# Optimization experiments

Measured on AMD Instinct MI355X. Metric: run time of the kernel, lower is better.

The kernel has to match this reference:

```python
import jax, jax.numpy as jnp
import numpy as np

B, N, DE, DH, L, DC = 8, 256, 768, 192, 2, 192
NEG = 1e30  # mask_logic constant from the repo


def setup_inputs() -> dict:
    ks = iter(jax.random.split(jax.random.key(0), 32))

    def nrm(shape, s=0.02):
        return jax.random.normal(next(ks), shape, dtype=jnp.float32) * s

    features = jax.random.normal(next(ks), (B, N, DE), dtype=jnp.float32)
    # DAG adjacency: node i attends to a subset of j < i; guarantee edge (i, i-1)
    rnd = jax.random.bernoulli(next(ks), 0.3, (B, N, N))
    tril = jnp.tril(jnp.ones((N, N), jnp.bool_), -1)
    adj = ((rnd & tril[None]) | jnp.eye(N, k=-1, dtype=jnp.bool_)[None]).astype(jnp.float32)
    s_mask = jax.random.bernoulli(next(ks), 0.5, (B, N, N)).astype(jnp.float32)
    s_mask_onehot = jnp.stack([1.0 - s_mask, s_mask], axis=-1)  # unused in forward
    lengths = jnp.full((B,), N, dtype=jnp.int32)  # unused (nodal_att_type=None)
    return dict(
        features=features, adj=adj, s_mask=s_mask,
        s_mask_onehot=s_mask_onehot, lengths=lengths,
        fc1_w=nrm((DE, DH)), fc1_b=jnp.zeros((DH,), jnp.float32),
        gat_w=nrm((L, 2 * DH)), gat_b=jnp.zeros((L,), jnp.float32),
        wr0=nrm((L, DH, DH)), wr1=nrm((L, DH, DH)),
        gruc_wih=nrm((L, 3 * DH, DH)), gruc_whh=nrm((L, 3 * DH, DH)),
        gruc_bih=jnp.zeros((L, 3 * DH), jnp.float32),
        gruc_bhh=jnp.zeros((L, 3 * DH), jnp.float32),
        grup_wih=nrm((L, 3 * DH, DH)), grup_whh=nrm((L, 3 * DH, DH)),
        grup_bih=jnp.zeros((L, 3 * DH), jnp.float32),
        grup_bhh=jnp.zeros((L, 3 * DH), jnp.float32),
        mlp_w0=nrm((DH * (L + 1), DH)), mlp_b0=jnp.zeros((DH,), jnp.float32),
        mlp_w1=nrm((DH, DH)), mlp_b1=jnp.zeros((DH,), jnp.float32),
        mlp_w2=nrm((DH, DC)), mlp_b2=jnp.zeros((DC,), jnp.float32),
    )


def _gru(x, h, wih, whh, bih, bhh):
    # torch.nn.GRUCell math
    gi = x @ wih.T + bih
    gh = h @ whh.T + bhh
    ir, iz, inn = jnp.split(gi, 3, axis=-1)
    hr, hz, hn = jnp.split(gh, 3, axis=-1)
    r = jax.nn.sigmoid(ir + hr)
    z = jax.nn.sigmoid(iz + hz)
    n = jnp.tanh(inn + r * hn)
    return (1.0 - z) * n + z * h


def _layer(Hl, adj, s_mask, gat_w, gat_b, wr0, wr1, cw, cp):
    # One DAG layer: sequential scan over nodes. Carry holds the relation-
    # projected value buffers V0=H1@Wr0^T, V1=H1@Wr1^T and per-node key
    # scores Ksc=H1@wk (rows >= i are zero and masked out), which is
    # mathematically identical to the torch code that re-projects the
    # growing H1 every step.
    wq, wk = gat_w[:DH], gat_w[DH:]
    pos = jnp.arange(N)

    def step(carry, xs):
        V0, V1, Ksc = carry
        i, x_i, adj_i, sm_i = xs  # x_i:(B,DH) adj_i,sm_i:(B,N)
        score = (x_i @ wq)[:, None] + Ksc + gat_b          # (B,N)
        mask = (pos < i)[None, :] & (adj_i > 0.5)          # ragged :i slice
        alpha = jnp.where(mask, score, score - NEG)        # mask_logic
        attn = jax.nn.softmax(alpha, axis=-1)              # masked -> exactly 0
        Vrel = V0 * sm_i[..., None] + V1 * (1.0 - sm_i[..., None])
        M = jnp.einsum('bn,bnd->bd', attn, Vrel)
        M = jnp.where(i > 0, M, 0.0)                       # node 0: no context
        C = _gru(x_i, M, *cw)
        P = _gru(M, x_i, *cp)
        Hnew = C + P
        V0 = V0.at[:, i, :].set(Hnew @ wr0.T)
        V1 = V1.at[:, i, :].set(Hnew @ wr1.T)
        Ksc = Ksc.at[:, i].set(Hnew @ wk)
        attn_out = jnp.where(i > 0, attn, 0.0)             # adjB row 0 is zeros
        return (V0, V1, Ksc), (Hnew, attn_out)

    z3 = jnp.zeros((B, N, DH), jnp.float32)
    carry0 = (z3, z3, jnp.zeros((B, N), jnp.float32))
    xs = (pos, Hl.transpose(1, 0, 2), adj.transpose(1, 0, 2), s_mask.transpose(1, 0, 2))
    _, (Hseq, Aseq) = jax.lax.scan(step, carry0, xs)
    return Hseq.transpose(1, 0, 2), Aseq.transpose(1, 0, 2)  # (B,N,DH),(B,N,N)


def reference(features, adj, s_mask, s_mask_onehot, lengths,
              fc1_w, fc1_b, gat_w, gat_b, wr0, wr1,
              gruc_wih, gruc_whh, gruc_bih, gruc_bhh,
              grup_wih, grup_whh, grup_bih, grup_bhh,
              mlp_w0, mlp_b0, mlp_w1, mlp_b1, mlp_w2, mlp_b2):
    Hl = jax.nn.relu(features @ fc1_w + fc1_b)  # H0
    Hs, As = [Hl], []
    for l in range(L):
        cw = (gruc_wih[l], gruc_whh[l], gruc_bih[l], gruc_bhh[l])
        cp = (grup_wih[l], grup_whh[l], grup_bih[l], grup_bhh[l])
        Hl, Al = _layer(Hl, adj, s_mask, gat_w[l], gat_b[l], wr0[l], wr1[l], cw, cp)
        Hs.append(Hl)
        As.append(Al)
    H = jnp.concatenate(Hs, axis=2)  # (B,N,DH*(L+1))
    # nodal_att_type=None => attentive_node_features is identity
    h = jax.nn.relu(H @ mlp_w0 + mlp_b0)
    h = jax.nn.relu(h @ mlp_w1 + mlp_b1)  # mlp_layers-1 = 1 extra block
    logits = h @ mlp_w2 + mlp_b2          # dropout: eval-mode identity
    return logits, jnp.stack(As, axis=1)  # (B,N,DC), (B,L,N,N)
```

## Files before the change

### kernel.cpp

```cpp
#include <hip/hip_runtime.h>
#include <stdint.h>

#define B_  8
#define N_  256
#define DH_ 192
#define L_  2
#define G3  576
#define G6  1152
#define NW  4
#define DS  48
#define KD  24
#define GC  288
#define STH 10001
#define STP 20001
#define STQ 25001

typedef unsigned long long u64;

__device__ __forceinline__ float bflo(uint32_t u) { return __uint_as_float(u << 16); }
__device__ __forceinline__ float bfhi(uint32_t u) { return __uint_as_float(u & 0xffff0000u); }
__device__ __forceinline__ uint32_t f2bf(float f) {
    uint32_t x = __float_as_uint(f);
    x += 0x7fffu + ((x >> 16) & 1u);
    return x >> 16;
}
__device__ __forceinline__ float sigm(float x)  { return 1.f / (1.f + __expf(-x)); }
__device__ __forceinline__ float tanhf_(float x){ return 1.f - 2.f / (1.f + __expf(2.f * x)); }
__device__ __forceinline__ u64 packvs(float v, int st) {
    return ((u64)(uint32_t)st << 32) | __float_as_uint(v);
}
__device__ __forceinline__ u64 agload(const u64* p) {
    return __hip_atomic_load(p, __ATOMIC_RELAXED, __HIP_MEMORY_SCOPE_AGENT);
}
__device__ __forceinline__ void agstore(u64* p, u64 v) {
    __hip_atomic_store(p, v, __ATOMIC_RELAXED, __HIP_MEMORY_SCOPE_AGENT);
}

__global__ void prepack_kernel(
    const float* __restrict__ wr0, const float* __restrict__ wr1,
    const float* __restrict__ c_wih, const float* __restrict__ c_whh,
    const float* __restrict__ c_bih, const float* __restrict__ c_bhh,
    const float* __restrict__ p_wih, const float* __restrict__ p_whh,
    const float* __restrict__ p_bih, const float* __restrict__ p_bhh,
    float* __restrict__ WpreT, uint32_t* __restrict__ W4,
    uint32_t* __restrict__ Wr4, uint32_t* __restrict__ Wp4w,
    float* __restrict__ biasPre, float* __restrict__ gbx)
{
    int idx = blockIdx.x * blockDim.x + threadIdx.x;
    if (idx >= DH_ * G6) return;
    for (int l = 0; l < L_; ++l) {
        const float* cwih = c_wih + l * G3 * DH_;
        const float* cwhh = c_whh + l * G3 * DH_;
        const float* pwih = p_wih + l * G3 * DH_;
        const float* pwhh = p_whh + l * G3 * DH_;
        if (l == 0) {
            int k = idx / G6, r = idx - k * G6;
            float w = (r < G3) ? cwih[r * DH_ + k] : pwhh[(r - G3) * DH_ + k];
            WpreT[k * G6 + r] = w;
        }
        if (idx < NW * 27648) {
            int w = idx / 27648, pos = idx % 27648;
            int p4 = pos / 1152, rem = pos % 1152;
            int c2 = rem >> 2, s = rem & 3;
            int p = 4 * p4 + s;
            int j = c2 / DS, dd = c2 % DS;
            int c = 192 * j + DS * w + dd;
            float w0 = (c < G3) ? cwhh[c * DH_ + 2 * p]     : pwih[(c - G3) * DH_ + 2 * p];
            float w1 = (c < G3) ? cwhh[c * DH_ + 2 * p + 1] : pwih[(c - G3) * DH_ + 2 * p + 1];
            W4[l * NW * 27648 + idx] = f2bf(w0) | (f2bf(w1) << 16);
            if (l == 1) {
                int r = 192 * j + DS * w + dd;
                float v0 = (r < G3) ? cwih[r * DH_ + 2 * p]     : pwhh[(r - G3) * DH_ + 2 * p];
                float v1 = (r < G3) ? cwih[r * DH_ + 2 * p + 1] : pwhh[(r - G3) * DH_ + 2 * p + 1];
                Wp4w[idx] = f2bf(v0) | (f2bf(v1) << 16);
            }
        }
        if (idx < NW * 9216) {
            int w = idx / 9216, pos = idx % 9216;
            int kq = pos / 768, rem = pos % 768;
            int d = rem >> 2, s = rem & 3;
            int k = DS * w + 4 * kq + s;
            Wr4[l * NW * 9216 + idx] =
                f2bf(wr0[l * DH_ * DH_ + d * DH_ + k]) |
                (f2bf(wr1[l * DH_ * DH_ + d * DH_ + k]) << 16);
        }
        if (idx < G6) {
            float base = (idx < G3) ? c_bih[l * G3 + idx] : p_bhh[l * G3 + idx - G3];
            float fold = 0.f;
            if (idx < 384)                    fold = c_bhh[l * G3 + idx];
            else if (idx >= G3 && idx < 960)  fold = p_bih[l * G3 + idx - G3];
            biasPre[l * G6 + idx] = base + fold;
        }
        if (idx < 384) {
            gbx[l * 384 + idx] = (idx < DH_) ? c_bhh[l * G3 + 384 + idx]
                                             : p_bih[l * G3 + 384 + (idx - DH_)];
        }
    }
}

#define GR 8
__global__ __launch_bounds__(192) void gemm_kernel(
    const float* __restrict__ A, int lda, const float* __restrict__ Bm,
    const float* __restrict__ bias, float* __restrict__ C, int ldc,
    int K, int cols, int relu)
{
    __shared__ float sA[GR][64];
    const int c  = blockIdx.y * 192 + threadIdx.x;
    const int r0 = blockIdx.x * GR;
    float acc[GR] = {0.f, 0.f, 0.f, 0.f, 0.f, 0.f, 0.f, 0.f};
    for (int k0 = 0; k0 < K; k0 += 64) {
        for (int idx = threadIdx.x; idx < GR * 64; idx += 192) {
            int rr = idx >> 6, kk = idx & 63;
            sA[rr][kk] = A[(size_t)(r0 + rr) * lda + k0 + kk];
        }
        __syncthreads();
        #pragma unroll 8
        for (int kk = 0; kk < 64; ++kk) {
            float bv = Bm[(size_t)(k0 + kk) * cols + c];
            #pragma unroll
            for (int rr = 0; rr < GR; ++rr) acc[rr] += sA[rr][kk] * bv;
        }
        __syncthreads();
    }
    float bv = bias[c];
    #pragma unroll
    for (int rr = 0; rr < GR; ++rr) {
        float v = acc[rr] + bv;
        if (relu) v = fmaxf(v, 0.f);
        C[(size_t)(r0 + rr) * ldc + c] = v;
    }
}

struct ScanSm {
    uint4 Wlds4[24 * GC];
    uint4 Wr4s[12 * DH_];
    float sA0[N_], sA1[N_], sKsc[N_];
    float sAdjN[N_], sSmN[N_];
    float sXq[DH_], sPre[6 * DS], sXv[DS];
    float sM[DH_], su0[DS], su1[DS], sGc[GC], sHn[DS];
    float sRedS[4], sRedX[3], sSaved[4];
};
struct WorkSm {
    uint4 Wp4[24 * GC];
    float sX[DH_];
    float sPv[GC];
    float sRed[3];
};

template<int ISL2>
__device__ void scan_body(
    ScanSm* S, int b, int w, int t,
    const float* __restrict__ xin, float* __restrict__ hout,
    const float* __restrict__ PREg, const float* __restrict__ adj,
    const float* __restrict__ smask,
    const uint32_t* __restrict__ W4l, const uint32_t* __restrict__ Wr4l,
    const float* __restrict__ gbxl, const float* __restrict__ gatwl,
    uint32_t* __restrict__ Hw, u64* __restrict__ MPsl, u64* __restrict__ Kdl,
    u64* __restrict__ HcW, const u64* __restrict__ HcR,
    const u64* __restrict__ PREcR, const u64* __restrict__ XQcR,
    float* __restrict__ AsB, int sbase)
{
    const int lane = t & 63, wave = t >> 6;
    const int dg0 = w * DS;
    const float* adjB = adj   + (size_t)b * N_ * N_;
    const float* smB  = smask + (size_t)b * N_ * N_;
    const int fi = b * NW;

    {
        uint32_t* wl = (uint32_t*)S->Wlds4;
        for (int q = t; q < 27648; q += 576) wl[q] = W4l[q];
        uint32_t* wr = (uint32_t*)S->Wr4s;
        for (int q = t; q < 9216; q += 576) wr[q] = Wr4l[q];
    }
    float wqv = (!ISL2 && t < DH_) ? gatwl[t] : 0.f;
    float wkv = 0.f, g2b = 0.f, g5b = 0.f;
    if (t < DS) { wkv = gatwl[DH_ + dg0 + t]; g2b = gbxl[dg0 + t]; g5b = gbxl[DH_ + dg0 + t]; }
    if (t < N_) S->sKsc[t] = 0.f;
    if (w == 0 && t < N_) AsB[t] = 0.f;

    if (!ISL2) {
        if (t < DS) {
            const float* pre = PREg + (size_t)(b * N_) * G6 + dg0 + t;
            S->sPre[t] = pre[0]; S->sPre[DS + t] = pre[192]; S->sPre[2 * DS + t] = pre[384];
            S->sPre[3 * DS + t] = pre[576]; S->sPre[4 * DS + t] = pre[768]; S->sPre[5 * DS + t] = pre[960];
            S->sXv[t] = xin[(size_t)(b * N_) * G3 + dg0 + t];
        }
        for (int q = t; q < 176; q += 576) {
            if (q < 64)       *(float4*)&S->sAdjN[4 * q] = *(const float4*)(adjB + N_ + 4 * q);
            else if (q < 128) { int q2 = q - 64;  *(float4*)&S->sSmN[4 * q2] = *(const float4*)(smB + N_ + 4 * q2); }
            else              { int q2 = q - 128; *(float4*)&S->sXq[4 * q2] = *(const float4*)(xin + (size_t)(b * N_ + 1) * G3 + 4 * q2); }
        }
    } else {
        for (int q = t; q < 321; q += 576) {
            if (q < 64)       *(float4*)&S->sAdjN[4 * q] = *(const float4*)(adjB + N_ + 4 * q);
            else if (q < 128) { int q2 = q - 64;  *(float4*)&S->sSmN[4 * q2] = *(const float4*)(smB + N_ + 4 * q2); }
            else if (q < 176) {
                int d = q - 128;
                const u64* p = HcR + ((size_t)(b * N_) * NW + w) * DS + d;
                u64 v; do { v = agload(p); } while ((uint32_t)(v >> 32) != (uint32_t)STH);
                S->sXv[d] = __uint_as_float((uint32_t)v);
            } else if (q < 320) {
                int qq = q - 176;
                const u64* p = PREcR + ((size_t)(b * N_) * NW + w) * 144 + qq;
                u64 v; do { v = agload(p); } while ((uint32_t)(v >> 32) != (uint32_t)STP);
                uint32_t pl = (uint32_t)v;
                S->sPre[2 * qq] = bflo(pl); S->sPre[2 * qq + 1] = bfhi(pl);
            } else {
                const u64* p = XQcR + b * N_ + 1;
                u64 v; do { v = agload(p); } while ((uint32_t)(v >> 32) != (uint32_t)(STQ + 1));
                S->sSaved[3] = __uint_as_float((uint32_t)v);
            }
        }
    }
    __syncthreads();
    {
        float hn = 0.f;
        if (t < DS) {
            float xv = S->sXv[t];
            float r1 = sigm(S->sPre[t]), z1 = sigm(S->sPre[DS + t]);
            float n1 = tanhf_(S->sPre[2 * DS + t] + r1 * g2b);
            float Cv = (1.f - z1) * n1;
            float r2 = sigm(S->sPre[3 * DS + t]), z2 = sigm(S->sPre[4 * DS + t]);
            float n2 = tanhf_(g5b + r2 * S->sPre[5 * DS + t]);
            hn = Cv + (1.f - z2) * n2 + z2 * xv;
            S->sHn[t] = hn;
            hout[(size_t)(b * N_) * G3 + dg0 + t] = hn;
            if (!ISL2) HcW[((size_t)(b * N_) * NW + w) * DS + t] = packvs(hn, STH);
        }
        if (wave == 0) {
            float v = hn * wkv;
            #pragma unroll
            for (int o = 32; o; o >>= 1) v += __shfl_xor(v, o);
            if (lane == 0) agstore(&Kdl[fi + w], packvs(v, sbase));
        }
    }
    __syncthreads();
    if (t < KD) Hw[(size_t)t * N_] = f2bf(S->sHn[2 * t]) | (f2bf(S->sHn[2 * t + 1]) << 16);
    if (!ISL2) {
        float px = (t < DH_) ? S->sXq[t] * wqv : 0.f;
        #pragma unroll
        for (int o = 32; o; o >>= 1) px += __shfl_xor(px, o);
        if (t < DH_ && lane == 0) S->sRedX[wave] = px;
    }
    __syncthreads();
    float xq = ISL2 ? S->sSaved[3] : (S->sRedX[0] + S->sRedX[1] + S->sRedX[2]);

    for (int i = 1; i < N_; ++i) {
        const int row = b * N_ + i;
        const int stamp = sbase + i;
        {
            float e = 0.f;
            if (t == i - 1) { S->sSaved[0] = S->sAdjN[t]; S->sSaved[1] = S->sSmN[t]; }
            if (t < N_) {
                if (t < i - 1 && S->sAdjN[t] > 0.5f) e = __expf(xq + S->sKsc[t]);
                float b0 = e * S->sSmN[t];
                S->sA0[t] = b0; S->sA1[t] = e - b0;
            }
            float ps = e;
            #pragma unroll
            for (int o = 32; o; o >>= 1) ps += __shfl_xor(ps, o);
            if (t < N_ && lane == 0) S->sRedS[wave] = ps;
        }
        __syncthreads();
        if (t < 384) {
            const int ilim = i - 1;
            const int kd = t >> 4, jp = t & 15;
            const uint32_t* hp = Hw + (size_t)kd * N_;
            float u0l = 0.f, u0h = 0.f, u1l = 0.f, u1h = 0.f;
            int j = jp;
            while (j + 48 < ilim) {
                uint32_t h0 = hp[j], h1 = hp[j + 16], h2 = hp[j + 32], h3 = hp[j + 48];
                float b0, b1;
                b0 = S->sA0[j];      b1 = S->sA1[j];
                u0l = fmaf(b0, bflo(h0), u0l); u0h = fmaf(b0, bfhi(h0), u0h);
                u1l = fmaf(b1, bflo(h0), u1l); u1h = fmaf(b1, bfhi(h0), u1h);
                b0 = S->sA0[j + 16]; b1 = S->sA1[j + 16];
                u0l = fmaf(b0, bflo(h1), u0l); u0h = fmaf(b0, bfhi(h1), u0h);
                u1l = fmaf(b1, bflo(h1), u1l); u1h = fmaf(b1, bfhi(h1), u1h);
                b0 = S->sA0[j + 32]; b1 = S->sA1[j + 32];
                u0l = fmaf(b0, bflo(h2), u0l); u0h = fmaf(b0, bfhi(h2), u0h);
                u1l = fmaf(b1, bflo(h2), u1l); u1h = fmaf(b1, bfhi(h2), u1h);
                b0 = S->sA0[j + 48]; b1 = S->sA1[j + 48];
                u0l = fmaf(b0, bflo(h3), u0l); u0h = fmaf(b0, bfhi(h3), u0h);
                u1l = fmaf(b1, bflo(h3), u1l); u1h = fmaf(b1, bfhi(h3), u1h);
                j += 64;
            }
            for (; j < ilim; j += 16) {
                uint32_t hv = hp[j];
                float b0 = S->sA0[j], b1 = S->sA1[j];
                u0l = fmaf(b0, bflo(hv), u0l); u0h = fmaf(b0, bfhi(hv), u0h);
                u1l = fmaf(b1, bflo(hv), u1l); u1h = fmaf(b1, bfhi(hv), u1h);
            }
            #pragma unroll
            for (int o = 1; o <= 8; o <<= 1) {
                u0l += __shfl_xor(u0l, o); u0h += __shfl_xor(u0h, o);
                u1l += __shfl_xor(u1l, o); u1h += __shfl_xor(u1h, o);
            }
            if (jp == 0) {
                S->su0[2 * kd] = u0l; S->su0[2 * kd + 1] = u0h;
                S->su1[2 * kd] = u1l; S->su1[2 * kd + 1] = u1h;
            }
        } else {
            const int u = t - 384;
            const int inx = (i + 1 < N_) ? i + 1 : N_ - 1;
            if (!ISL2) {
                for (int q = u; q < 260; q += 192) {
                    if (q < 64)
                        *(float4*)&S->sAdjN[4 * q] = *(const float4*)(adjB + (size_t)inx * N_ + 4 * q);
                    else if (q < 128) { int q2 = q - 64;
                        *(float4*)&S->sSmN[4 * q2] = *(const float4*)(smB + (size_t)inx * N_ + 4 * q2); }
                    else if (q < 140) { int q2 = q - 128;
                        *(float4*)&S->sXv[4 * q2] = *(const float4*)(xin + (size_t)row * G3 + dg0 + 4 * q2); }
                    else if (q < 212) { int q2 = q - 140; int g = q2 / 12, o = q2 - 12 * g;
                        *(float4*)&S->sPre[g * DS + 4 * o] =
                            *(const float4*)(PREg + (size_t)row * G6 + g * DH_ + dg0 + 4 * o); }
                    else { int q2 = q - 212;
                        *(float4*)&S->sXq[4 * q2] = *(const float4*)(xin + (size_t)(b * N_ + inx) * G3 + 4 * q2); }
                }
            } else {
                for (int q = u; q < 321; q += 192) {
                    if (q < 64)
                        *(float4*)&S->sAdjN[4 * q] = *(const float4*)(adjB + (size_t)inx * N_ + 4 * q);
                    else if (q < 128) { int q2 = q - 64;
                        *(float4*)&S->sSmN[4 * q2] = *(const float4*)(smB + (size_t)inx * N_ + 4 * q2); }
                    else if (q < 176) {
                        int d = q - 128;
                        const u64* p = HcR + ((size_t)row * NW + w) * DS + d;
                        u64 v; do { v = agload(p); } while ((uint32_t)(v >> 32) != (uint32_t)(STH + i));
                        S->sXv[d] = __uint_as_float((uint32_t)v);
                    } else if (q < 320) {
                        int qq = q - 176;
                        const u64* p = PREcR + ((size_t)row * NW + w) * 144 + qq;
                        u64 v; do { v = agload(p); } while ((uint32_t)(v >> 32) != (uint32_t)(STP + i));
                        uint32_t pl = (uint32_t)v;
                        S->sPre[2 * qq] = bflo(pl); S->sPre[2 * qq + 1] = bfhi(pl);
                    } else {
                        const u64* p = XQcR + b * N_ + inx;
                        u64 v; do { v = agload(p); } while ((uint32_t)(v >> 32) != (uint32_t)(STQ + inx));
                        S->sSaved[3] = __uint_as_float((uint32_t)v);
                    }
                }
            }
            if (t == 575) {
                const uint32_t ex = (uint32_t)(stamp - 1);
                u64 k0, k1, k2, k3;
                do {
                    k0 = agload(&Kdl[fi + 0]); k1 = agload(&Kdl[fi + 1]);
                    k2 = agload(&Kdl[fi + 2]); k3 = agload(&Kdl[fi + 3]);
                } while ((uint32_t)(k0 >> 32) != ex || (uint32_t)(k1 >> 32) != ex ||
                         (uint32_t)(k2 >> 32) != ex || (uint32_t)(k3 >> 32) != ex);
                float kdot = __uint_as_float((uint32_t)k0) + __uint_as_float((uint32_t)k1)
                           + __uint_as_float((uint32_t)k2) + __uint_as_float((uint32_t)k3);
                float adjI1 = S->sSaved[0], smI1 = S->sSaved[1];
                float e1 = (adjI1 > 0.5f) ? __expf(xq + kdot) : 0.f;
                float Ssum = S->sRedS[0] + S->sRedS[1] + S->sRedS[2] + S->sRedS[3] + e1;
                S->sKsc[i - 1] = kdot;
                float c0 = e1 * smI1;
                S->sA0[i - 1] = c0; S->sA1[i - 1] = e1 - c0;
                S->sSaved[2] = 1.f / Ssum;
            }
        }
        __syncthreads();
        if (t < DH_) {
            float mp = 0.f, h0a = 0.f, h1a = 0.f;
            #pragma unroll 4
            for (int kq = 0; kq < 12; ++kq) {
                uint4 wv = S->Wr4s[kq * DH_ + t];
                const int k0 = 4 * kq;
                float lo, hi;
                lo = bflo(wv.x); hi = bfhi(wv.x);
                mp = fmaf(S->su0[k0 + 0], lo, mp); mp = fmaf(S->su1[k0 + 0], hi, mp);
                h0a = fmaf(S->sHn[k0 + 0], lo, h0a); h1a = fmaf(S->sHn[k0 + 0], hi, h1a);
                lo = bflo(wv.y); hi = bfhi(wv.y);
                mp = fmaf(S->su0[k0 + 1], lo, mp); mp = fmaf(S->su1[k0 + 1], hi, mp);
                h0a = fmaf(S->sHn[k0 + 1], lo, h0a); h1a = fmaf(S->sHn[k0 + 1], hi, h1a);
                lo = bflo(wv.z); hi = bfhi(wv.z);
                mp = fmaf(S->su0[k0 + 2], lo, mp); mp = fmaf(S->su1[k0 + 2], hi, mp);
                h0a = fmaf(S->sHn[k0 + 2], lo, h0a); h1a = fmaf(S->sHn[k0 + 2], hi, h1a);
                lo = bflo(wv.w); hi = bfhi(wv.w);
                mp = fmaf(S->su0[k0 + 3], lo, mp); mp = fmaf(S->su1[k0 + 3], hi, mp);
                h0a = fmaf(S->sHn[k0 + 3], lo, h0a); h1a = fmaf(S->sHn[k0 + 3], hi, h1a);
            }
            float invS = S->sSaved[2];
            mp = (mp + S->sA0[i - 1] * h0a + S->sA1[i - 1] * h1a) * invS;
            agstore(&MPsl[(size_t)(fi + w) * DH_ + t], packvs(mp, stamp));
            const int w1 = (w + 1) & 3, w2 = (w + 2) & 3, w3 = (w + 3) & 3;
            u64* pA = &MPsl[(size_t)(fi + w1) * DH_ + t];
            u64* pB = &MPsl[(size_t)(fi + w2) * DH_ + t];
            u64* pC = &MPsl[(size_t)(fi + w3) * DH_ + t];
            const uint32_t ex = (uint32_t)stamp;
            u64 vA, vB, vC;
            do {
                vA = agload(pA); vB = agload(pB); vC = agload(pC);
            } while ((uint32_t)(vA >> 32) != ex || (uint32_t)(vB >> 32) != ex ||
                     (uint32_t)(vC >> 32) != ex);
            S->sM[t] = mp + __uint_as_float((uint32_t)vA)
                          + __uint_as_float((uint32_t)vB)
                          + __uint_as_float((uint32_t)vC);
        } else if (w == 0 && t < 448) {
            int j = t - 192;
            AsB[(size_t)i * N_ + j] = (S->sA0[j] + S->sA1[j]) * S->sSaved[2];
        }
        __syncthreads();
        {
            const int c = t >> 1, kh = t & 1;
            const uint4* wp = S->Wlds4 + (12 * kh) * GC + c;
            float g = 0.f;
            #pragma unroll 4
            for (int p4 = 0; p4 < 12; ++p4) {
                uint4 wv = wp[p4 * GC];
                const int m0 = 8 * (12 * kh + p4);
                g = fmaf(S->sM[m0 + 0], bflo(wv.x), g); g = fmaf(S->sM[m0 + 1], bfhi(wv.x), g);
                g = fmaf(S->sM[m0 + 2], bflo(wv.y), g); g = fmaf(S->sM[m0 + 3], bfhi(wv.y), g);
                g = fmaf(S->sM[m0 + 4], bflo(wv.z), g); g = fmaf(S->sM[m0 + 5], bfhi(wv.z), g);
                g = fmaf(S->sM[m0 + 6], bflo(wv.w), g); g = fmaf(S->sM[m0 + 7], bfhi(wv.w), g);
            }
            g += __shfl_xor(g, 1);
            if (kh == 0) S->sGc[c] = g;
        }
        __syncthreads();
        {
            float hn = 0.f;
            if (t < DS) {
                float Mv = S->sM[dg0 + t];
                float r1 = sigm(S->sPre[t] + S->sGc[t]);
                float z1 = sigm(S->sPre[DS + t] + S->sGc[DS + t]);
                float n1 = tanhf_(S->sPre[2 * DS + t] + r1 * (S->sGc[2 * DS + t] + g2b));
                float Cv = (1.f - z1) * n1 + z1 * Mv;
                float r2 = sigm(S->sGc[3 * DS + t] + S->sPre[3 * DS + t]);
                float z2 = sigm(S->sGc[4 * DS + t] + S->sPre[4 * DS + t]);
                float n2 = tanhf_(S->sGc[5 * DS + t] + g5b + r2 * S->sPre[5 * DS + t]);
                hn = Cv + (1.f - z2) * n2 + z2 * S->sXv[t];
                S->sHn[t] = hn;
                hout[(size_t)row * G3 + dg0 + t] = hn;
                if (!ISL2) HcW[((size_t)row * NW + w) * DS + t] = packvs(hn, STH + i);
            }
            if (wave == 0) {
                float v = hn * wkv;
                #pragma unroll
                for (int o = 32; o; o >>= 1) v += __shfl_xor(v, o);
                if (lane == 0) agstore(&Kdl[fi + w], packvs(v, stamp));
            }
            if (t < KD) Hw[(size_t)t * N_ + i] = f2bf(S->sHn[2 * t]) | (f2bf(S->sHn[2 * t + 1]) << 16);
            if (!ISL2) {
                float px = (t < DH_) ? S->sXq[t] * wqv : 0.f;
                #pragma unroll
                for (int o = 32; o; o >>= 1) px += __shfl_xor(px, o);
                if (t < DH_ && lane == 0) S->sRedX[wave] = px;
            }
        }
        __syncthreads();
        xq = ISL2 ? S->sSaved[3] : (S->sRedX[0] + S->sRedX[1] + S->sRedX[2]);
    }
}

__device__ void worker_body(WorkSm* Wm, int b, int w, int t,
    const uint32_t* __restrict__ Wp4g, const float* __restrict__ bias2,
    const float* __restrict__ wq2,
    const u64* __restrict__ HcR, u64* __restrict__ PREcW, u64* __restrict__ XQcW)
{
    const int lane = t & 63, wave = t >> 6;
    { uint32_t* wl = (uint32_t*)Wm->Wp4; for (int q = t; q < 27648; q += 576) wl[q] = Wp4g[q]; }
    const int c = t >> 1, kh = t & 1;
    float bv = 0.f;
    if (kh == 0) bv = bias2[192 * (c / DS) + w * DS + (c % DS)];
    float wqt = (t < DH_) ? wq2[t] : 0.f;
    for (int i = 0; i < N_; ++i) {
        if (t < DH_) {
            const u64* p = HcR + ((size_t)(b * N_ + i) * NW + (t / DS)) * DS + (t % DS);
            u64 v; do { v = agload(p); } while ((uint32_t)(v >> 32) != (uint32_t)(STH + i));
            Wm->sX[t] = __uint_as_float((uint32_t)v);
        }
        __syncthreads();
        {
            const uint4* wp = Wm->Wp4 + (12 * kh) * GC + c;
            float g = 0.f;
            #pragma unroll 4
            for (int p4 = 0; p4 < 12; ++p4) {
                uint4 wv = wp[p4 * GC];
                const int m0 = 8 * (12 * kh + p4);
                g = fmaf(Wm->sX[m0 + 0], bflo(wv.x), g); g = fmaf(Wm->sX[m0 + 1], bfhi(wv.x), g);
                g = fmaf(Wm->sX[m0 + 2], bflo(wv.y), g); g = fmaf(Wm->sX[m0 + 3], bfhi(wv.y), g);
                g = fmaf(Wm->sX[m0 + 4], bflo(wv.z), g); g = fmaf(Wm->sX[m0 + 5], bfhi(wv.z), g);
                g = fmaf(Wm->sX[m0 + 6], bflo(wv.w), g); g = fmaf(Wm->sX[m0 + 7], bfhi(wv.w), g);
            }
            g += __shfl_xor(g, 1);
            if (kh == 0) Wm->sPv[c] = g + bv;
        }
        if (w == 0) {
            float px = (t < DH_) ? Wm->sX[t] * wqt : 0.f;
            #pragma unroll
            for (int o = 32; o; o >>= 1) px += __shfl_xor(px, o);
            if (t < DH_ && lane == 0) Wm->sRed[wave] = px;
        }
        __syncthreads();
        if (t < 144) {
            u64 v = ((u64)(uint32_t)(STP + i) << 32)
                  | f2bf(Wm->sPv[2 * t]) | (f2bf(Wm->sPv[2 * t + 1]) << 16);
            agstore(&PREcW[((size_t)(b * N_ + i) * NW + w) * 144 + t], v);
        }
        if (w == 0 && t == 0)
            agstore(&XQcW[b * N_ + i],
                    packvs(Wm->sRed[0] + Wm->sRed[1] + Wm->sRed[2], STQ + i));
        __syncthreads();
    }
}

__global__ __launch_bounds__(576, 1) void pipeline_kernel(
    float* __restrict__ Hcat, const float* __restrict__ PREg,
    const float* __restrict__ adj, const float* __restrict__ smask,
    const uint32_t* __restrict__ W4, const uint32_t* __restrict__ Wr4,
    const uint32_t* __restrict__ Wp4w,
    const float* __restrict__ biasPre, const float* __restrict__ gbx,
    const float* __restrict__ gatw,
    uint32_t* __restrict__ Hb, u64* __restrict__ MPs, u64* __restrict__ Kd,
    u64* __restrict__ Hc, u64* __restrict__ PREc, u64* __restrict__ XQc,
    float* __restrict__ As)
{
    __shared__ __align__(16) char smem[sizeof(ScanSm)];
    const int blk = blockIdx.x, t = threadIdx.x;
    const int b = blk & 7, r12 = blk >> 3;
    const int role = r12 >> 2, w = r12 & 3;
    if (role == 0) {
        scan_body<0>((ScanSm*)smem, b, w, t,
            Hcat, Hcat + 192, PREg, adj, smask,
            W4, Wr4, gbx, gatw,
            Hb + (size_t)(b * NW + w) * KD * N_, MPs, Kd,
            Hc, nullptr, nullptr, nullptr,
            As + (size_t)b * (L_ * N_ * N_), 1);
    } else if (role == 2) {
        scan_body<1>((ScanSm*)smem, b, w, t,
            nullptr, Hcat + 384, nullptr, adj, smask,
            W4 + NW * 27648, Wr4 + NW * 9216, gbx + 384, gatw + 384,
            Hb + (size_t)(32 + b * NW + w) * KD * N_,
            MPs + (size_t)8 * NW * DH_, Kd + 8 * NW,
            nullptr, Hc, PREc, XQc,
            As + (size_t)b * (L_ * N_ * N_) + N_ * N_, 30001);
    } else {
        worker_body((WorkSm*)smem, b, w, t,
            Wp4w + (size_t)w * 27648, biasPre + G6, gatw + 384,
            Hc, PREc, XQc);
    }
}

extern "C" void kernel_launch(void* const* d_in, const int* in_sizes, int n_in,
                              void* d_out, int out_size, void* d_ws, size_t ws_size,
                              hipStream_t stream)
{
    const float* features = (const float*)d_in[0];
    const float* adj      = (const float*)d_in[1];
    const float* smask    = (const float*)d_in[2];
    const float* fc1_w = (const float*)d_in[5];
    const float* fc1_b = (const float*)d_in[6];
    const float* gat_w = (const float*)d_in[7];
    const float* wr0   = (const float*)d_in[9];
    const float* wr1   = (const float*)d_in[10];
    const float* c_wih = (const float*)d_in[11];
    const float* c_whh = (const float*)d_in[12];
    const float* c_bih = (const float*)d_in[13];
    const float* c_bhh = (const float*)d_in[14];
    const float* p_wih = (const float*)d_in[15];
    const float* p_whh = (const float*)d_in[16];
    const float* p_bih = (const float*)d_in[17];
    const float* p_bhh = (const float*)d_in[18];
    const float* mw0 = (const float*)d_in[19];
    const float* mb0 = (const float*)d_in[20];
    const float* mw1 = (const float*)d_in[21];
    const float* mb1 = (const float*)d_in[22];
    const float* mw2 = (const float*)d_in[23];
    const float* mb2 = (const float*)d_in[24];
    float* out = (float*)d_out;

    char* wsb = (char*)d_ws;
    size_t off = 0;
    auto carve = [&](size_t bytes) -> char* {
        char* p = wsb + off;
        off = (off + bytes + 255) & ~(size_t)255;
        return p;
    };
    float* Hcat     = (float*)carve(2048ull * 576 * 4);
    float* PREg     = (float*)carve(2048ull * 1152 * 4);
    float* WpreT    = (float*)carve(192ull * 1152 * 4);
    uint32_t* W4    = (uint32_t*)carve(2ull * NW * 27648 * 4);
    uint32_t* Wr4   = (uint32_t*)carve(2ull * NW * 9216 * 4);
    uint32_t* Wp4w  = (uint32_t*)carve((size_t)NW * 27648 * 4);
    float* biasPre  = (float*)carve(2ull * 1152 * 4);
    float* gbx      = (float*)carve(2ull * 384 * 4);
    uint32_t* Hb    = (uint32_t*)carve(64ull * KD * 256 * 4);
    u64* MPs        = (u64*)carve(2ull * 8 * NW * DH_ * 8);
    u64* Kd         = (u64*)carve(2ull * 8 * NW * 8);
    u64* Hc         = (u64*)carve(8ull * 256 * NW * DS * 8);
    u64* PREc       = (u64*)carve(8ull * 256 * NW * 144 * 8);
    u64* XQc        = (u64*)carve(8ull * 256 * 8);
    float* h1 = PREg;
    float* h2 = PREg + 2048 * 192;

    prepack_kernel<<<dim3((192 * 1152 + 255) / 256), 256, 0, stream>>>(
        wr0, wr1, c_wih, c_whh, c_bih, c_bhh, p_wih, p_whh, p_bih, p_bhh,
        WpreT, W4, Wr4, Wp4w, biasPre, gbx);

    gemm_kernel<<<dim3(256, 1), 192, 0, stream>>>(features, 768, fc1_w, fc1_b,
                                                  Hcat, 576, 768, 192, 1);
    gemm_kernel<<<dim3(256, 6), 192, 0, stream>>>(Hcat, 576,
        WpreT, biasPre, PREg, 1152, 192, 1152, 0);

    pipeline_kernel<<<dim3(96), 576, 0, stream>>>(
        Hcat, PREg, adj, smask, W4, Wr4, Wp4w, biasPre, gbx, gat_w,
        Hb, MPs, Kd, Hc, PREc, XQc, out + 393216);

    gemm_kernel<<<dim3(256, 1), 192, 0, stream>>>(Hcat, 576, mw0, mb0, h1, 192, 576, 192, 1);
    gemm_kernel<<<dim3(256, 1), 192, 0, stream>>>(h1, 192, mw1, mb1, h2, 192, 192, 192, 1);
    gemm_kernel<<<dim3(256, 1), 192, 0, stream>>>(h2, 192, mw2, mb2, out, 192, 192, 192, 0);
}
```

Before: 2.006 ms.

## Fuse prepack, prologue GEMMs and MLP tail into single persistent pipeline kernel

Merges the weight-prepack kernel, the fc1 and pre-activation GEMMs, and the three MLP GEMMs into the persistent 96-block pipeline kernel. Phases are separated by software grid barriers built on stamped flags in global memory. The MLP tail waits on per-scan completion flags. The goal is to remove five kernel launches and their gaps, at the cost of spin-wait grid barriers that need all 96 blocks resident at once, and GEMMs that now run on only 96 workgroups.

```diff
diff --git a/kernel.cpp b/kernel.cpp
--- a/kernel.cpp
+++ b/kernel.cpp
@@ -14,6 +14,10 @@
 #define STH 10001
 #define STP 20001
 #define STQ 25001
+#define SPK 50000
+#define SF1 50001
+#define SF2 50002
+#define SDN 60001
 
 typedef unsigned long long u64;
 
@@ -34,101 +38,6 @@
 }
 __device__ __forceinline__ void agstore(u64* p, u64 v) {
     __hip_atomic_store(p, v, __ATOMIC_RELAXED, __HIP_MEMORY_SCOPE_AGENT);
-}
-
-__global__ void prepack_kernel(
-    const float* __restrict__ wr0, const float* __restrict__ wr1,
-    const float* __restrict__ c_wih, const float* __restrict__ c_whh,
-    const float* __restrict__ c_bih, const float* __restrict__ c_bhh,
-    const float* __restrict__ p_wih, const float* __restrict__ p_whh,
-    const float* __restrict__ p_bih, const float* __restrict__ p_bhh,
-    float* __restrict__ WpreT, uint32_t* __restrict__ W4,
-    uint32_t* __restrict__ Wr4, uint32_t* __restrict__ Wp4w,
-    float* __restrict__ biasPre, float* __restrict__ gbx)
-{
-    int idx = blockIdx.x * blockDim.x + threadIdx.x;
-    if (idx >= DH_ * G6) return;
-    for (int l = 0; l < L_; ++l) {
-        const float* cwih = c_wih + l * G3 * DH_;
-        const float* cwhh = c_whh + l * G3 * DH_;
-        const float* pwih = p_wih + l * G3 * DH_;
-        const float* pwhh = p_whh + l * G3 * DH_;
-        if (l == 0) {
-            int k = idx / G6, r = idx - k * G6;
-            float w = (r < G3) ? cwih[r * DH_ + k] : pwhh[(r - G3) * DH_ + k];
-            WpreT[k * G6 + r] = w;
-        }
-        if (idx < NW * 27648) {
-            int w = idx / 27648, pos = idx % 27648;
-            int p4 = pos / 1152, rem = pos % 1152;
-            int c2 = rem >> 2, s = rem & 3;
-            int p = 4 * p4 + s;
-            int j = c2 / DS, dd = c2 % DS;
-            int c = 192 * j + DS * w + dd;
-            float w0 = (c < G3) ? cwhh[c * DH_ + 2 * p]     : pwih[(c - G3) * DH_ + 2 * p];
-            float w1 = (c < G3) ? cwhh[c * DH_ + 2 * p + 1] : pwih[(c - G3) * DH_ + 2 * p + 1];
-            W4[l * NW * 27648 + idx] = f2bf(w0) | (f2bf(w1) << 16);
-            if (l == 1) {
-                int r = 192 * j + DS * w + dd;
-                float v0 = (r < G3) ? cwih[r * DH_ + 2 * p]     : pwhh[(r - G3) * DH_ + 2 * p];
-                float v1 = (r < G3) ? cwih[r * DH_ + 2 * p + 1] : pwhh[(r - G3) * DH_ + 2 * p + 1];
-                Wp4w[idx] = f2bf(v0) | (f2bf(v1) << 16);
-            }
-        }
-        if (idx < NW * 9216) {
-            int w = idx / 9216, pos = idx % 9216;
-            int kq = pos / 768, rem = pos % 768;
-            int d = rem >> 2, s = rem & 3;
-            int k = DS * w + 4 * kq + s;
-            Wr4[l * NW * 9216 + idx] =
-                f2bf(wr0[l * DH_ * DH_ + d * DH_ + k]) |
-                (f2bf(wr1[l * DH_ * DH_ + d * DH_ + k]) << 16);
-        }
-        if (idx < G6) {
-            float base = (idx < G3) ? c_bih[l * G3 + idx] : p_bhh[l * G3 + idx - G3];
-            float fold = 0.f;
-            if (idx < 384)                    fold = c_bhh[l * G3 + idx];
-            else if (idx >= G3 && idx < 960)  fold = p_bih[l * G3 + idx - G3];
-            biasPre[l * G6 + idx] = base + fold;
-        }
-        if (idx < 384) {
-            gbx[l * 384 + idx] = (idx < DH_) ? c_bhh[l * G3 + 384 + idx]
-                                             : p_bih[l * G3 + 384 + (idx - DH_)];
-        }
-    }
-}
-
-#define GR 8
-__global__ __launch_bounds__(192) void gemm_kernel(
-    const float* __restrict__ A, int lda, const float* __restrict__ Bm,
-    const float* __restrict__ bias, float* __restrict__ C, int ldc,
-    int K, int cols, int relu)
-{
-    __shared__ float sA[GR][64];
-    const int c  = blockIdx.y * 192 + threadIdx.x;
-    const int r0 = blockIdx.x * GR;
-    float acc[GR] = {0.f, 0.f, 0.f, 0.f, 0.f, 0.f, 0.f, 0.f};
-    for (int k0 = 0; k0 < K; k0 += 64) {
-        for (int idx = threadIdx.x; idx < GR * 64; idx += 192) {
-            int rr = idx >> 6, kk = idx & 63;
-            sA[rr][kk] = A[(size_t)(r0 + rr) * lda + k0 + kk];
-        }
-        __syncthreads();
-        #pragma unroll 8
-        for (int kk = 0; kk < 64; ++kk) {
-            float bv = Bm[(size_t)(k0 + kk) * cols + c];
-            #pragma unroll
-            for (int rr = 0; rr < GR; ++rr) acc[rr] += sA[rr][kk] * bv;
-        }
-        __syncthreads();
-    }
-    float bv = bias[c];
-    #pragma unroll
-    for (int rr = 0; rr < GR; ++rr) {
-        float v = acc[rr] + bv;
-        if (relu) v = fmaxf(v, 0.f);
-        C[(size_t)(r0 + rr) * ldc + c] = v;
-    }
 }
 
 struct ScanSm {
@@ -146,6 +55,248 @@
     float sPv[GC];
     float sRed[3];
 };
+struct PrologSm {
+    float sA[8][768];
+    float sRed[3][8][192];
+};
+struct MlpSm {
+    float sH[8][576];
+    float sRed[3][8][192];
+    float sT[8][192];
+};
+
+__device__ void prepack_slice(int idx,
+    const float* __restrict__ wr0, const float* __restrict__ wr1,
+    const float* __restrict__ c_wih, const float* __restrict__ c_whh,
+    const float* __restrict__ c_bih, const float* __restrict__ c_bhh,
+    const float* __restrict__ p_wih, const float* __restrict__ p_whh,
+    const float* __restrict__ p_bih, const float* __restrict__ p_bhh,
+    float* __restrict__ WpreT, uint32_t* __restrict__ W4,
+    uint32_t* __restrict__ Wr4, uint32_t* __restrict__ Wp4w,
+    float* __restrict__ biasPre, float* __restrict__ gbx)
+{
+    for (int l = 0; l < L_; ++l) {
+        const float* cwih = c_wih + l * G3 * DH_;
+        const float* cwhh = c_whh + l * G3 * DH_;
+        const float* pwih = p_wih + l * G3 * DH_;
+        const float* pwhh = p_whh + l * G3 * DH_;
+        if (l == 0) {
+            int k = idx / G6, r = idx - k * G6;
+            float w = (r < G3) ? cwih[r * DH_ + k] : pwhh[(r - G3) * DH_ + k];
+            WpreT[k * G6 + r] = w;
+        }
+        if (idx < NW * 27648) {
+            int w = idx / 27648, pos = idx % 27648;
+            int p4 = pos / 1152, rem = pos % 1152;
+            int c2 = rem >> 2, s = rem & 3;
+            int p = 4 * p4 + s;
+            int j = c2 / DS, dd = c2 % DS;
+            int c = 192 * j + DS * w + dd;
+            float w0 = (c < G3) ? cwhh[c * DH_ + 2 * p]     : pwih[(c - G3) * DH_ + 2 * p];
+            float w1 = (c < G3) ? cwhh[c * DH_ + 2 * p + 1] : pwih[(c - G3) * DH_ + 2 * p + 1];
+            W4[l * NW * 27648 + idx] = f2bf(w0) | (f2bf(w1) << 16);
+            if (l == 1) {
+                int r = c;
+                float v0 = (r < G3) ? cwih[r * DH_ + 2 * p]     : pwhh[(r - G3) * DH_ + 2 * p];
+                float v1 = (r < G3) ? cwih[r * DH_ + 2 * p + 1] : pwhh[(r - G3) * DH_ + 2 * p + 1];
+                Wp4w[idx] = f2bf(v0) | (f2bf(v1) << 16);
+            }
+        }
+        if (idx < NW * 9216) {
+            int w = idx / 9216, pos = idx % 9216;
+            int kq = pos / 768, rem = pos % 768;
+            int d = rem >> 2, s = rem & 3;
+            int k = DS * w + 4 * kq + s;
+            Wr4[l * NW * 9216 + idx] =
+                f2bf(wr0[l * DH_ * DH_ + d * DH_ + k]) |
+                (f2bf(wr1[l * DH_ * DH_ + d * DH_ + k]) << 16);
+        }
+        if (idx < G6) {
+            float base = (idx < G3) ? c_bih[l * G3 + idx] : p_bhh[l * G3 + idx - G3];
+            float fold = 0.f;
+            if (idx < 384)                    fold = c_bhh[l * G3 + idx];
+            else if (idx >= G3 && idx < 960)  fold = p_bih[l * G3 + idx - G3];
+            biasPre[l * G6 + idx] = base + fold;
+        }
+        if (idx < 384) {
+            gbx[l * 384 + idx] = (idx < DH_) ? c_bhh[l * G3 + 384 + idx]
+                                             : p_bih[l * G3 + 384 + (idx - DH_)];
+        }
+    }
+}
+
+__device__ void flag_sync(u64* flags, int wgid, int t, int stamp)
+{
+    __threadfence();
+    __syncthreads();
+    if (t == 0) agstore(&flags[wgid], packvs(0.f, stamp));
+    if (t < 96) {
+        while ((uint32_t)(agload(&flags[t]) >> 32) != (uint32_t)stamp) {}
+    }
+    __syncthreads();
+    __threadfence();
+    __syncthreads();
+}
+
+__device__ void prologue(char* smem, int wgid, int t,
+    const float* __restrict__ features, const float* __restrict__ fc1_w,
+    const float* __restrict__ fc1_b, const float* __restrict__ WpreT,
+    const float* __restrict__ biasPre,
+    float* __restrict__ Hcat, float* __restrict__ PREg, u64* __restrict__ Fp)
+{
+    PrologSm* P = (PrologSm*)smem;
+    const int c = t % 192, kg = t / 192;
+    for (int tt = wgid; tt < 256; tt += 96) {
+        const int r0 = tt * 8;
+        for (int q = t; q < 1536; q += 576) {
+            int r = q / 192, c4 = q % 192;
+            *(float4*)&P->sA[r][4 * c4] = *(const float4*)(features + (size_t)(r0 + r) * 768 + 4 * c4);
+        }
+        __syncthreads();
+        {
+            const float* bp = fc1_w + (size_t)(kg * 256) * 192 + c;
+            float acc[8] = {0.f, 0.f, 0.f, 0.f, 0.f, 0.f, 0.f, 0.f};
+            #pragma unroll 8
+            for (int kk = 0; kk < 256; ++kk) {
+                float bv = bp[(size_t)kk * 192];
+                #pragma unroll
+                for (int rr = 0; rr < 8; ++rr) acc[rr] += P->sA[rr][kg * 256 + kk] * bv;
+            }
+            #pragma unroll
+            for (int rr = 0; rr < 8; ++rr) P->sRed[kg][rr][c] = acc[rr];
+        }
+        __syncthreads();
+        if (t < 192) {
+            float bv = fc1_b[t];
+            #pragma unroll
+            for (int rr = 0; rr < 8; ++rr) {
+                float v = P->sRed[0][rr][t] + P->sRed[1][rr][t] + P->sRed[2][rr][t] + bv;
+                Hcat[(size_t)(r0 + rr) * G3 + t] = fmaxf(v, 0.f);
+            }
+        }
+        __syncthreads();
+    }
+    flag_sync(Fp + 96, wgid, t, SF1);
+    {
+        const float bpa = biasPre[t], bpb = biasPre[576 + t];
+        for (int tt = wgid; tt < 256; tt += 96) {
+            const int r0 = tt * 8;
+            for (int q = t; q < 384; q += 576) {
+                int r = q / 48, c4 = q % 48;
+                *(float4*)&P->sA[r][4 * c4] = *(const float4*)(Hcat + (size_t)(r0 + r) * G3 + 4 * c4);
+            }
+            __syncthreads();
+            {
+                const float* b0 = WpreT + t;
+                float a0[8] = {0.f,0.f,0.f,0.f,0.f,0.f,0.f,0.f};
+                float a1[8] = {0.f,0.f,0.f,0.f,0.f,0.f,0.f,0.f};
+                #pragma unroll 4
+                for (int k = 0; k < 192; ++k) {
+                    float bva = b0[(size_t)k * G6];
+                    float bvb = b0[(size_t)k * G6 + 576];
+                    #pragma unroll
+                    for (int rr = 0; rr < 8; ++rr) {
+                        float av = P->sA[rr][k];
+                        a0[rr] += av * bva; a1[rr] += av * bvb;
+                    }
+                }
+                #pragma unroll
+                for (int rr = 0; rr < 8; ++rr) {
+                    PREg[(size_t)(r0 + rr) * G6 + t]       = a0[rr] + bpa;
+                    PREg[(size_t)(r0 + rr) * G6 + 576 + t] = a1[rr] + bpb;
+                }
+            }
+            __syncthreads();
+        }
+    }
+    flag_sync(Fp + 192, wgid, t, SF2);
+}
+
+__device__ void mlp_tail(char* smem, int wgid, int t,
+    const float* __restrict__ Hcat,
+    const float* __restrict__ mw0, const float* __restrict__ mb0,
+    const float* __restrict__ mw1, const float* __restrict__ mb1,
+    const float* __restrict__ mw2, const float* __restrict__ mb2,
+    float* __restrict__ out, u64* __restrict__ Fd)
+{
+    if (t < 64) {
+        while ((uint32_t)(agload(&Fd[t]) >> 32) != (uint32_t)SDN) {}
+    }
+    __syncthreads();
+    __threadfence();
+    __syncthreads();
+    MlpSm* M = (MlpSm*)smem;
+    const int c = t % 192, kg = t / 192;
+    for (int tt = wgid; tt < 256; tt += 96) {
+        const int r0 = tt * 8;
+        for (int q = t; q < 1152; q += 576) {
+            int r = q / 144, c4 = q % 144;
+            *(float4*)&M->sH[r][4 * c4] = *(const float4*)(Hcat + (size_t)(r0 + r) * G3 + 4 * c4);
+        }
+        __syncthreads();
+        {
+            const float* bp = mw0 + (size_t)(kg * 192) * 192 + c;
+            float acc[8] = {0.f,0.f,0.f,0.f,0.f,0.f,0.f,0.f};
+            #pragma unroll 8
+            for (int kk = 0; kk < 192; ++kk) {
+                float bv = bp[(size_t)kk * 192];
+                #pragma unroll
+                for (int rr = 0; rr < 8; ++rr) acc[rr] += M->sH[rr][kg * 192 + kk] * bv;
+            }
+            #pragma unroll
+            for (int rr = 0; rr < 8; ++rr) M->sRed[kg][rr][c] = acc[rr];
+        }
+        __syncthreads();
+        if (t < 192) {
+            float bv = mb0[t];
+            #pragma unroll
+            for (int rr = 0; rr < 8; ++rr)
+                M->sT[rr][t] = fmaxf(M->sRed[0][rr][t] + M->sRed[1][rr][t] + M->sRed[2][rr][t] + bv, 0.f);
+        }
+        __syncthreads();
+        {
+            const float* bp = mw1 + (size_t)(kg * 64) * 192 + c;
+            float acc[8] = {0.f,0.f,0.f,0.f,0.f,0.f,0.f,0.f};
+            #pragma unroll 8
+            for (int kk = 0; kk < 64; ++kk) {
+                float bv = bp[(size_t)kk * 192];
+                #pragma unroll
+                for (int rr = 0; rr < 8; ++rr) acc[rr] += M->sT[rr][kg * 64 + kk] * bv;
+            }
+            #pragma unroll
+            for (int rr = 0; rr < 8; ++rr) M->sRed[kg][rr][c] = acc[rr];
+        }
+        __syncthreads();
+        if (t < 192) {
+            float bv = mb1[t];
+            #pragma unroll
+            for (int rr = 0; rr < 8; ++rr)
+                M->sH[rr][t] = fmaxf(M->sRed[0][rr][t] + M->sRed[1][rr][t] + M->sRed[2][rr][t] + bv, 0.f);
+        }
+        __syncthreads();
+        {
+            const float* bp = mw2 + (size_t)(kg * 64) * 192 + c;
+            float acc[8] = {0.f,0.f,0.f,0.f,0.f,0.f,0.f,0.f};
+            #pragma unroll 8
+            for (int kk = 0; kk < 64; ++kk) {
+                float bv = bp[(size_t)kk * 192];
+                #pragma unroll
+                for (int rr = 0; rr < 8; ++rr) acc[rr] += M->sH[rr][kg * 64 + kk] * bv;
+            }
+            #pragma unroll
+            for (int rr = 0; rr < 8; ++rr) M->sRed[kg][rr][c] = acc[rr];
+        }
+        __syncthreads();
+        if (t < 192) {
+            float bv = mb2[t];
+            #pragma unroll
+            for (int rr = 0; rr < 8; ++rr)
+                out[(size_t)(r0 + rr) * 192 + t] =
+                    M->sRed[0][rr][t] + M->sRed[1][rr][t] + M->sRed[2][rr][t] + bv;
+        }
+        __syncthreads();
+    }
+}
 
 template<int ISL2>
 __device__ void scan_body(
@@ -507,20 +658,45 @@
 }
 
 __global__ __launch_bounds__(576, 1) void pipeline_kernel(
-    float* __restrict__ Hcat, const float* __restrict__ PREg,
+    const float* __restrict__ features, const float* __restrict__ fc1_w,
+    const float* __restrict__ fc1_b,
     const float* __restrict__ adj, const float* __restrict__ smask,
-    const uint32_t* __restrict__ W4, const uint32_t* __restrict__ Wr4,
-    const uint32_t* __restrict__ Wp4w,
-    const float* __restrict__ biasPre, const float* __restrict__ gbx,
     const float* __restrict__ gatw,
+    const float* __restrict__ wr0, const float* __restrict__ wr1,
+    const float* __restrict__ c_wih, const float* __restrict__ c_whh,
+    const float* __restrict__ c_bih, const float* __restrict__ c_bhh,
+    const float* __restrict__ p_wih, const float* __restrict__ p_whh,
+    const float* __restrict__ p_bih, const float* __restrict__ p_bhh,
+    const float* __restrict__ mw0, const float* __restrict__ mb0,
+    const float* __restrict__ mw1, const float* __restrict__ mb1,
+    const float* __restrict__ mw2, const float* __restrict__ mb2,
+    float* __restrict__ Hcat, float* __restrict__ PREg,
+    float* __restrict__ WpreT, uint32_t* __restrict__ W4,
+    uint32_t* __restrict__ Wr4, uint32_t* __restrict__ Wp4w,
+    float* __restrict__ biasPre, float* __restrict__ gbx,
     uint32_t* __restrict__ Hb, u64* __restrict__ MPs, u64* __restrict__ Kd,
     u64* __restrict__ Hc, u64* __restrict__ PREc, u64* __restrict__ XQc,
-    float* __restrict__ As)
+    u64* __restrict__ Fp, u64* __restrict__ Fd,
+    float* __restrict__ out)
 {
     __shared__ __align__(16) char smem[sizeof(ScanSm)];
     const int blk = blockIdx.x, t = threadIdx.x;
+    const int wgid = blk;
     const int b = blk & 7, r12 = blk >> 3;
     const int role = r12 >> 2, w = r12 & 3;
+
+    for (int j = 0; j < 4; ++j) {
+        int idx = wgid * 576 + t + 55296 * j;
+        prepack_slice(idx, wr0, wr1, c_wih, c_whh, c_bih, c_bhh,
+                      p_wih, p_whh, p_bih, p_bhh,
+                      WpreT, W4, Wr4, Wp4w, biasPre, gbx);
+    }
+    flag_sync(Fp, wgid, t, SPK);
+
+    prologue(smem, wgid, t, features, fc1_w, fc1_b, WpreT, biasPre,
+             Hcat, PREg, Fp);
+
+    float* As = out + 393216;
     if (role == 0) {
         scan_body<0>((ScanSm*)smem, b, w, t,
             Hcat, Hcat + 192, PREg, adj, smask,
@@ -528,6 +704,9 @@
             Hb + (size_t)(b * NW + w) * KD * N_, MPs, Kd,
             Hc, nullptr, nullptr, nullptr,
             As + (size_t)b * (L_ * N_ * N_), 1);
+        __threadfence();
+        __syncthreads();
+        if (t == 0) agstore(&Fd[b * 8 + w], packvs(0.f, SDN));
     } else if (role == 2) {
         scan_body<1>((ScanSm*)smem, b, w, t,
             nullptr, Hcat + 384, nullptr, adj, smask,
@@ -536,11 +715,16 @@
             MPs + (size_t)8 * NW * DH_, Kd + 8 * NW,
             nullptr, Hc, PREc, XQc,
             As + (size_t)b * (L_ * N_ * N_) + N_ * N_, 30001);
+        __threadfence();
+        __syncthreads();
+        if (t == 0) agstore(&Fd[b * 8 + 4 + w], packvs(0.f, SDN));
     } else {
         worker_body((WorkSm*)smem, b, w, t,
             Wp4w + (size_t)w * 27648, biasPre + G6, gatw + 384,
             Hc, PREc, XQc);
     }
+
+    mlp_tail(smem, wgid, t, Hcat, mw0, mb0, mw1, mb1, mw2, mb2, out, Fd);
 }
 
 extern "C" void kernel_launch(void* const* d_in, const int* in_sizes, int n_in,
@@ -592,23 +776,13 @@
     u64* Hc         = (u64*)carve(8ull * 256 * NW * DS * 8);
     u64* PREc       = (u64*)carve(8ull * 256 * NW * 144 * 8);
     u64* XQc        = (u64*)carve(8ull * 256 * 8);
-    float* h1 = PREg;
-    float* h2 = PREg + 2048 * 192;
-
-    prepack_kernel<<<dim3((192 * 1152 + 255) / 256), 256, 0, stream>>>(
+    u64* Fp         = (u64*)carve(288ull * 8);
+    u64* Fd         = (u64*)carve(64ull * 8);
+
+    pipeline_kernel<<<dim3(96), 576, 0, stream>>>(
+        features, fc1_w, fc1_b, adj, smask, gat_w,
         wr0, wr1, c_wih, c_whh, c_bih, c_bhh, p_wih, p_whh, p_bih, p_bhh,
-        WpreT, W4, Wr4, Wp4w, biasPre, gbx);
-
-    gemm_kernel<<<dim3(256, 1), 192, 0, stream>>>(features, 768, fc1_w, fc1_b,
-                                                  Hcat, 576, 768, 192, 1);
-    gemm_kernel<<<dim3(256, 6), 192, 0, stream>>>(Hcat, 576,
-        WpreT, biasPre, PREg, 1152, 192, 1152, 0);
-
-    pipeline_kernel<<<dim3(96), 576, 0, stream>>>(
-        Hcat, PREg, adj, smask, W4, Wr4, Wp4w, biasPre, gbx, gat_w,
-        Hb, MPs, Kd, Hc, PREc, XQc, out + 393216);
-
-    gemm_kernel<<<dim3(256, 1), 192, 0, stream>>>(Hcat, 576, mw0, mb0, h1, 192, 576, 192, 1);
-    gemm_kernel<<<dim3(256, 1), 192, 0, stream>>>(h1, 192, mw1, mb1, h2, 192, 192, 192, 1);
-    gemm_kernel<<<dim3(256, 1), 192, 0, stream>>>(h2, 192, mw2, mb2, out, 192, 192, 192, 0);
-}
+        mw0, mb0, mw1, mb1, mw2, mb2,
+        Hcat, PREg, WpreT, W4, Wr4, Wp4w, biasPre, gbx,
+        Hb, MPs, Kd, Hc, PREc, XQc, Fp, Fd, out);
+}
```

Measured after the change: 1.932 ms. 1.04x faster.
